# Kernel optimization log

Hardware: AMD Instinct MI355X
Metric: run time of the kernel (lower is better)

Reference implementation:

```python
import jax, jax.numpy as jnp
import numpy as np

N_NODES = 100000
N_EDGES = 1600000
NUM_FEATURES = 64
HIDDEN = 64
NUM_CLASSES = 16


def setup_inputs() -> dict:
    key = jax.random.key(0)
    ks = jax.random.split(key, 8)
    x = jax.random.normal(ks[0], (N_NODES, NUM_FEATURES), dtype=jnp.float32)
    edge_index = jax.random.randint(ks[1], (2, N_EDGES), 0, N_NODES, dtype=jnp.int32)
    # Glorot-ish init for weights, zero bias (matches GCNConv / Linear defaults closely enough)
    s1 = 1.0 / np.sqrt(NUM_FEATURES)
    s2 = 1.0 / np.sqrt(HIDDEN)
    W1 = jax.random.uniform(ks[2], (NUM_FEATURES, HIDDEN), jnp.float32, -s1, s1)
    b1 = jnp.zeros((HIDDEN,), jnp.float32)
    W2 = jax.random.uniform(ks[3], (HIDDEN, HIDDEN), jnp.float32, -s2, s2)
    b2 = jnp.zeros((HIDDEN,), jnp.float32)
    W3 = jax.random.uniform(ks[4], (HIDDEN, NUM_CLASSES), jnp.float32, -s2, s2)
    b3 = jax.random.uniform(ks[5], (NUM_CLASSES,), jnp.float32, -s2, s2)
    return {"x": x, "edge_index": edge_index, "W1": W1, "b1": b1,
            "W2": W2, "b2": b2, "W3": W3, "b3": b3}


def _gcn_layer(x, W, b, src, dst, norm, n_nodes):
    # GCNConv: h = X W; out[i] = sum_{(j->i)} norm_ji * h[j]; out += b
    h = x @ W                                   # [N, H] small dense GEMM
    msg = h[src] * norm[:, None]                # [E+N, H] irregular gather
    out = jax.ops.segment_sum(msg, dst, num_segments=n_nodes)  # scatter-add
    return out + b


def reference(x, edge_index, W1, b1, W2, b2, W3, b3):
    n = x.shape[0]
    loop = jnp.arange(n, dtype=edge_index.dtype)
    # add self-loops (PyG GCNConv default add_self_loops=True)
    src = jnp.concatenate([edge_index[0], loop])
    dst = jnp.concatenate([edge_index[1], loop])
    # symmetric normalization D^{-1/2} A_hat D^{-1/2}
    deg = jax.ops.segment_sum(jnp.ones_like(src, dtype=x.dtype), dst, num_segments=n)
    dis = jax.lax.rsqrt(deg)                    # deg >= 1 due to self-loops
    norm = dis[src] * dis[dst]                  # [E+N]

    h = jax.nn.relu(_gcn_layer(x, W1, b1, src, dst, norm, n))
    # F.dropout(training=False) -> identity (module in eval mode)
    h = jax.nn.relu(_gcn_layer(h, W2, b2, src, dst, norm, n))
    z = h @ W3 + b3
    return jax.nn.log_softmax(z, axis=1), h
```

## Files before the change

kernel.cpp:

```cpp
#include <hip/hip_runtime.h>
#include <hip/hip_bf16.h>

typedef __hip_bfloat16 bf16;
typedef unsigned short ushort;

#define NN 100000
#define NE 1600000
#define NBKT 391
#define BCAP 4608
#define EPB 4096
#define NP1 391
#define NMT 6250

typedef __attribute__((ext_vector_type(8))) short s8v;
typedef __attribute__((ext_vector_type(4))) float f4v;
typedef __attribute__((ext_vector_type(2))) float f2v;

__device__ __forceinline__ float ldf(const void* p, int i, int f32) {
    return f32 ? ((const float*)p)[i] : __bfloat162float(((const bf16*)p)[i]);
}
__device__ __forceinline__ void stf(void* p, int i, int f32, float v) {
    if (f32) ((float*)p)[i] = v;
    else     ((bf16*)p)[i] = __float2bfloat16(v);
}

__device__ __forceinline__ ushort f2b(float f) {
    unsigned u = __builtin_bit_cast(unsigned, f);
    u += 0x7FFF + ((u >> 16) & 1);
    return (ushort)(u >> 16);
}
__device__ __forceinline__ float b2f(ushort h) {
    unsigned u = ((unsigned)h) << 16;
    return __builtin_bit_cast(float, u);
}
__device__ __forceinline__ float blo(unsigned u) {
    return __builtin_bit_cast(float, u << 16);
}
__device__ __forceinline__ float bhi(unsigned u) {
    return __builtin_bit_cast(float, u & 0xffff0000u);
}
__device__ __forceinline__ f2v up2(unsigned u) {
    f2v r; r.x = blo(u); r.y = bhi(u); return r;
}

__global__ void k_sentinel(unsigned* out) {
    if (threadIdx.x == 0 && blockIdx.x == 0) out[0] = 0x461C461Cu;
}

__global__ void k_cnt(const unsigned* __restrict__ x, int* __restrict__ flag,
                      const int* __restrict__ dst, int* __restrict__ cnt) {
    __shared__ int hist[NBKT];
    int b = blockIdx.x, t = threadIdx.x;
    for (int i = t; i < NBKT; i += 256) hist[i] = 0;
    __syncthreads();
    int e0 = b * EPB;
#pragma unroll
    for (int k = 0; k < EPB; k += 256) {
        int e = e0 + k + t;
        if (e < NE) atomicAdd(&hist[dst[e] >> 8], 1);
    }
    __syncthreads();
    for (int i = t; i < NBKT; i += 256) cnt[b * NBKT + i] = hist[i];
    if (b == 0) {
        int c = 0;
        for (int i = t; i < 2048; i += 256) {
            unsigned e7 = (x[i] >> 8) & 0x7F;
            c += (e7 >= 60 && e7 <= 66) ? 1 : 0;
        }
        __syncthreads();
        hist[t] = c;
        __syncthreads();
        for (int s = 128; s > 0; s >>= 1) {
            if (t < s) hist[t] += hist[t + s];
            __syncthreads();
        }
        if (t == 0) *flag = (hist[0] >= 1024) ? 0 : 1;
    }
}

__global__ void k_colscan(const int* __restrict__ cnt, int* __restrict__ prefT,
                          int* __restrict__ btot) {
    __shared__ int s[512];
    int k = blockIdx.x, t = threadIdx.x;
    int v = (t < NP1) ? cnt[t * NBKT + k] : 0;
    s[t] = v;
    __syncthreads();
    for (int d = 1; d < 512; d <<= 1) {
        int add = (t >= d) ? s[t - d] : 0;
        __syncthreads();
        s[t] += add;
        __syncthreads();
    }
    if (t < NP1) prefT[k * NP1 + t] = s[t] - v;
    if (t == 511) btot[k] = s[511];
}

__global__ void __launch_bounds__(512) k_place(
        const int* __restrict__ src, const int* __restrict__ dst,
        const int* __restrict__ prefT, unsigned* __restrict__ bbuf) {
    __shared__ int base[NBKT];
    __shared__ int hist[NBKT];
    __shared__ int lofs[512];
    __shared__ unsigned vals[EPB];
    __shared__ int addr[EPB];
    int b = blockIdx.x, t = threadIdx.x;
    for (int i = t; i < NBKT; i += 512) {
        base[i] = prefT[i * NP1 + b];
        hist[i] = 0;
    }
    __syncthreads();
    int e0 = b * EPB;
    unsigned ev[8];
    int kb[8];
#pragma unroll
    for (int k = 0; k < 8; k++) {
        int e = e0 + k * 512 + t;
        if (e < NE) {
            int d = dst[e];
            ev[k] = ((unsigned)src[e] << 8) | (unsigned)(d & 255);
            kb[k] = d >> 8;
        } else kb[k] = -1;
    }
#pragma unroll
    for (int k = 0; k < 8; k++)
        if (kb[k] >= 0) atomicAdd(&hist[kb[k]], 1);
    __syncthreads();
    int v = (t < NBKT) ? hist[t] : 0;
    lofs[t] = v;
    __syncthreads();
    for (int d = 1; d < 512; d <<= 1) {
        int add = (t >= d) ? lofs[t - d] : 0;
        __syncthreads();
        lofs[t] += add;
        __syncthreads();
    }
    int ex = lofs[t] - v;
    __syncthreads();
    lofs[t] = ex;
    if (t < NBKT) hist[t] = 0;
    __syncthreads();
#pragma unroll
    for (int k = 0; k < 8; k++) {
        if (kb[k] >= 0) {
            int p = atomicAdd(&hist[kb[k]], 1);
            int li = lofs[kb[k]] + p;
            vals[li] = ev[k];
            addr[li] = kb[k] * BCAP + base[kb[k]] + p;
        }
    }
    __syncthreads();
    int tot = min(EPB, NE - e0);
    for (int i = t; i < tot; i += 512) bbuf[addr[i]] = vals[i];
}

__global__ void k_pass2(const unsigned* __restrict__ bbuf, const int* __restrict__ btot,
                        int* __restrict__ rowptr, float* __restrict__ dis,
                        int* __restrict__ csr_off) {
    __shared__ unsigned vals[BCAP];
    __shared__ int lout[BCAP];
    __shared__ int fh[256], fx[256], fc[256];
    int b = blockIdx.x, t = threadIdx.x;
    int part = 0;
    for (int i = t; i < b; i += 256) part += btot[i];
    fh[t] = part;
    __syncthreads();
    for (int s = 128; s > 0; s >>= 1) {
        if (t < s) fh[t] += fh[t + s];
        __syncthreads();
    }
    int g0 = fh[0];
    int cntb = btot[b];
    if (b == 0 && t == 0) rowptr[NN] = NE;
    __syncthreads();
    const unsigned* in = bbuf + b * BCAP;
    fh[t] = 0;
    __syncthreads();
    for (int i = t; i < cntb; i += 256) {
        unsigned v = in[i];
        vals[i] = v;
        atomicAdd(&fh[v & 255], 1);
    }
    __syncthreads();
    fx[t] = fh[t];
    __syncthreads();
    for (int d = 1; d < 256; d <<= 1) {
        int add = (t >= d) ? fx[t - d] : 0;
        __syncthreads();
        fx[t] += add;
        __syncthreads();
    }
    int n = b * 256 + t;
    int ex = fx[t] - fh[t];
    fc[t] = ex;
    if (n < NN) {
        rowptr[n] = g0 + ex;
        dis[n] = rsqrtf(1.0f + (float)fh[t]);
    }
    __syncthreads();
    for (int i = t; i < cntb; i += 256) {
        unsigned v = vals[i];
        int p = atomicAdd(&fc[v & 255], 1);
        lout[p] = (int)((v >> 8) << 7);
    }
    __syncthreads();
    for (int i = t; i < cntb; i += 256) csr_off[g0 + i] = lout[i];
}

__global__ void __launch_bounds__(256) k_gemm_mfma(
        const void* __restrict__ A, int aBase, const void* __restrict__ W,
        bf16* __restrict__ C, const float* __restrict__ dis,
        const int* __restrict__ flag) {
    int f32 = *flag;
    int t = threadIdx.x;
    if (blockIdx.x == 0 && t < 64) ((ushort*)C)[NN * 64 + t] = 0;
    int lane = t & 63;
    int w = t >> 6;
    int m = lane & 15, q = lane >> 4;

    s8v bh[2][4], bl[2][4];
#pragma unroll
    for (int st = 0; st < 2; st++)
#pragma unroll
        for (int nt = 0; nt < 4; nt++)
#pragma unroll
            for (int j = 0; j < 8; j++) {
                int k = st * 32 + q * 8 + j;
                float wv = ldf(W, k * 64 + nt * 16 + m, f32);
                ushort h = f2b(wv);
                bh[st][nt][j] = (short)h;
                bl[st][nt][j] = (short)f2b(wv - b2f(h));
            }

    ushort* Cu = (ushort*)C;
    int gw = blockIdx.x * 4 + w;
    int nw = gridDim.x * 4;
    for (int mt = gw; mt < NMT; mt += nw) {
        int row = mt * 16 + m;
        s8v ah[2], al[2];
        if (f32) {
            const float* ap = (const float*)A + aBase + row * 64 + q * 8;
#pragma unroll
            for (int st = 0; st < 2; st++) {
                f4v va = *(const f4v*)(ap + st * 32);
                f4v vb = *(const f4v*)(ap + st * 32 + 4);
#pragma unroll
                for (int j = 0; j < 8; j++) {
                    float v = (j < 4) ? va[j] : vb[j - 4];
                    ushort h = f2b(v);
                    ah[st][j] = (short)h;
                    al[st][j] = (short)f2b(v - b2f(h));
                }
            }
        } else {
            const short* ap = (const short*)A + aBase + row * 64 + q * 8;
            ah[0] = *(const s8v*)(ap);
            ah[1] = *(const s8v*)(ap + 32);
        }
        float dr[4];
#pragma unroll
        for (int r = 0; r < 4; r++) dr[r] = dis[mt * 16 + q * 4 + r];
#pragma unroll
        for (int nt = 0; nt < 4; nt++) {
            f4v acc = {0.f, 0.f, 0.f, 0.f};
#pragma unroll
            for (int st = 0; st < 2; st++)
                acc = __builtin_amdgcn_mfma_f32_16x16x32_bf16(ah[st], bh[st][nt], acc, 0, 0, 0);
            if (f32) {
#pragma unroll
                for (int st = 0; st < 2; st++) {
                    acc = __builtin_amdgcn_mfma_f32_16x16x32_bf16(ah[st], bl[st][nt], acc, 0, 0, 0);
                    acc = __builtin_amdgcn_mfma_f32_16x16x32_bf16(al[st], bh[st][nt], acc, 0, 0, 0);
                }
            }
            int col = nt * 16 + m;
#pragma unroll
            for (int r = 0; r < 4; r++) {
                int rr = mt * 16 + q * 4 + r;
                Cu[rr * 64 + col] = f2b(dr[r] * acc[r]);
            }
        }
    }
}

__global__ void __launch_bounds__(256, 8) k_aggregate(
        const bf16* __restrict__ hs, void* hout, int hoBase,
        const float* __restrict__ dis,
        const int* __restrict__ rowptr,
        const int* __restrict__ csr_off,
        const void* __restrict__ bias,
        const int* __restrict__ flag) {
    int f32 = *flag;
    int t = threadIdx.x;
    int l = t & 63;
    int q = l >> 4;
    int m = l & 15;
    int fb = m * 8;
    const char* hb = (const char*)hs;
    float b0 = ldf(bias, m * 4 + 0, f32);
    float b1v = ldf(bias, m * 4 + 1, f32);
    float b2v = ldf(bias, m * 4 + 2, f32);
    float b3v = ldf(bias, m * 4 + 3, f32);
    const int Z = NN * 128;
    int wid = blockIdx.x * 4 + (t >> 6);
    int nwav = gridDim.x * 4;
    for (int n = wid; n < NN; n += nwav) {
        int r0 = rowptr[n], r1 = rowptr[n + 1];
        f2v a01 = {0.f, 0.f}, a23 = {0.f, 0.f};
        int j = r0;
        for (; j + 16 <= r1; j += 16) {
            int o0 = csr_off[j + q];
            int o1 = csr_off[j + 4 + q];
            int o2 = csr_off[j + 8 + q];
            int o3 = csr_off[j + 12 + q];
            uint2 v0 = *(const uint2*)(hb + o0 + fb);
            uint2 v1 = *(const uint2*)(hb + o1 + fb);
            uint2 v2 = *(const uint2*)(hb + o2 + fb);
            uint2 v3 = *(const uint2*)(hb + o3 + fb);
            a01 += up2(v0.x); a23 += up2(v0.y);
            a01 += up2(v1.x); a23 += up2(v1.y);
            a01 += up2(v2.x); a23 += up2(v2.y);
            a01 += up2(v3.x); a23 += up2(v3.y);
        }
        if (j < r1) {
            int i0 = j + q, i1 = j + 4 + q, i2 = j + 8 + q, i3 = j + 12 + q;
            int o0 = csr_off[i0]; o0 = (i0 < r1) ? o0 : Z;
            int o1 = csr_off[i1]; o1 = (i1 < r1) ? o1 : Z;
            int o2 = csr_off[i2]; o2 = (i2 < r1) ? o2 : Z;
            int o3 = csr_off[i3]; o3 = (i3 < r1) ? o3 : Z;
            uint2 v0 = *(const uint2*)(hb + o0 + fb);
            uint2 v1 = *(const uint2*)(hb + o1 + fb);
            uint2 v2 = *(const uint2*)(hb + o2 + fb);
            uint2 v3 = *(const uint2*)(hb + o3 + fb);
            a01 += up2(v0.x); a23 += up2(v0.y);
            a01 += up2(v1.x); a23 += up2(v1.y);
            a01 += up2(v2.x); a23 += up2(v2.y);
            a01 += up2(v3.x); a23 += up2(v3.y);
        }
        float a0 = a01.x, a1 = a01.y, a2 = a23.x, a3 = a23.y;
        a0 += __shfl_xor(a0, 32); a1 += __shfl_xor(a1, 32);
        a2 += __shfl_xor(a2, 32); a3 += __shfl_xor(a3, 32);
        a0 += __shfl_xor(a0, 16); a1 += __shfl_xor(a1, 16);
        a2 += __shfl_xor(a2, 16); a3 += __shfl_xor(a3, 16);
        if (q == 0) {
            uint2 sv = *(const uint2*)(hb + n * 128 + fb);
            float dn = dis[n];
            float o0 = fmaxf(dn * (a0 + blo(sv.x)) + b0, 0.f);
            float o1 = fmaxf(dn * (a1 + bhi(sv.x)) + b1v, 0.f);
            float o2 = fmaxf(dn * (a2 + blo(sv.y)) + b2v, 0.f);
            float o3 = fmaxf(dn * (a3 + bhi(sv.y)) + b3v, 0.f);
            if (f32) {
                float4 ov = {o0, o1, o2, o3};
                *(float4*)((float*)hout + hoBase + n * 64 + m * 4) = ov;
            } else {
                unsigned w0 = (unsigned)f2b(o0) | ((unsigned)f2b(o1) << 16);
                unsigned w1 = (unsigned)f2b(o2) | ((unsigned)f2b(o3) << 16);
                uint2 wv; wv.x = w0; wv.y = w1;
                *(uint2*)((ushort*)hout + hoBase + n * 64 + m * 4) = wv;
            }
        }
    }
}

__global__ void k_head(const void* __restrict__ h2, int hBase,
                       const void* __restrict__ W3, const void* __restrict__ b3,
                       void* out, const int* __restrict__ flag) {
    __shared__ float w[64 * 16];
    __shared__ float hrow[64 * 65];
    int f32 = *flag;
    int t = threadIdx.x;
#pragma unroll
    for (int i = 0; i < 4; i++) w[t + i * 256] = ldf(W3, t + i * 256, f32);
    int r0 = blockIdx.x * 64;
#pragma unroll
    for (int i = 0; i < 16; i++) {
        int idx = t + i * 256;
        int row = idx >> 6;
        hrow[row * 65 + (idx & 63)] =
            (r0 + row < NN) ? ldf(h2, hBase + r0 * 64 + idx, f32) : 0.f;
    }
    __syncthreads();
    int lr = t >> 4, c = t & 15;
    float bc = ldf(b3, c, f32);
#pragma unroll
    for (int g = 0; g < 4; g++) {
        int row = lr + g * 16;
        float z = bc;
#pragma unroll
        for (int k = 0; k < 64; k++) z += hrow[row * 65 + k] * w[k * 16 + c];
        float m = z;
#pragma unroll
        for (int off = 8; off >= 1; off >>= 1) m = fmaxf(m, __shfl_xor(m, off, 16));
        float p = __expf(z - m);
        float s = p;
#pragma unroll
        for (int off = 8; off >= 1; off >>= 1) s += __shfl_xor(s, off, 16);
        if (r0 + row < NN)
            stf(out, (r0 + row) * 16 + c, f32, z - m - __logf(s));
    }
}

extern "C" void kernel_launch(void* const* d_in, const int* in_sizes, int n_in,
                              void* d_out, int out_size, void* d_ws, size_t ws_size,
                              hipStream_t stream) {
    const void* x  = d_in[0];
    const int* ei  = (const int*)d_in[1];
    const void* W1 = d_in[2];
    const void* b1 = d_in[3];
    const void* W2 = d_in[4];
    const void* b2 = d_in[5];
    const void* W3 = d_in[6];
    const void* b3 = d_in[7];

    const size_t NEEDED = (size_t)(1807104 + 3203072) * 4;
    if (ws_size < NEEDED) {
        k_sentinel<<<1, 64, 0, stream>>>((unsigned*)d_out);
        return;
    }
    int*      flag    = (int*)d_ws;
    float*    dis     = (float*)d_ws + 256;
    int*      rowptr  = (int*)d_ws + 102656;
    int*      btot    = (int*)d_ws + 205568;
    int*      csr_off = (int*)d_ws + 207104;
    unsigned* bbuf    = (unsigned*)((int*)d_ws + 1807104);
    int*      cnt     = (int*)d_ws + 1807104 + NBKT * BCAP;
    int*      prefT   = cnt + 153088;
    bf16*     bufA    = (bf16*)bbuf;

    const int* srcp = ei;
    const int* dstp = ei + NE;
    const int HB = NN * 16;

    k_cnt<<<NP1, 256, 0, stream>>>((const unsigned*)x, flag, dstp, cnt);
    k_colscan<<<NBKT, 512, 0, stream>>>(cnt, prefT, btot);
    k_place<<<NP1, 512, 0, stream>>>(srcp, dstp, prefT, bbuf);
    k_pass2<<<NBKT, 256, 0, stream>>>(bbuf, btot, rowptr, dis, csr_off);

    k_gemm_mfma<<<1563, 256, 0, stream>>>(x, 0, W1, bufA, dis, flag);
    k_aggregate<<<2048, 256, 0, stream>>>(bufA, d_out, HB, dis, rowptr,
                                          csr_off, b1, flag);

    k_gemm_mfma<<<1563, 256, 0, stream>>>(d_out, HB, W2, bufA, dis, flag);
    k_aggregate<<<2048, 256, 0, stream>>>(bufA, d_out, HB, dis, rowptr,
                                          csr_off, b2, flag);

    k_head<<<1563, 256, 0, stream>>>(d_out, HB, W3, b3, d_out, flag);
}
```

Baseline: 258.0 us.

## Fuse CSR build kernels into one cooperative kernel with grid syncs

Merges the four CSR-construction kernels (count, column scan, place, pass2) into a single cooperative kernel of 391 blocks by 512 threads, using grid.sync() between phases and one shared-memory arena reused across phases. This removes three kernel launches and their inter-kernel gaps. In exchange it adds grid-wide barrier cost, depends on all 391 blocks being co-resident, and runs the count and pass2 phases at 512 threads where they previously used 256.

Result: slower. 406.9 us (+57.7%).

```diff
diff --git a/kernel.cpp b/kernel.cpp
--- a/kernel.cpp
+++ b/kernel.cpp
@@ -1,5 +1,8 @@
 #include <hip/hip_runtime.h>
 #include <hip/hip_bf16.h>
+#include <hip/hip_cooperative_groups.h>
+
+namespace cg = cooperative_groups;
 
 typedef __hip_bfloat16 bf16;
 typedef unsigned short ushort;
@@ -47,163 +50,169 @@
     if (threadIdx.x == 0 && blockIdx.x == 0) out[0] = 0x461C461Cu;
 }
 
-__global__ void k_cnt(const unsigned* __restrict__ x, int* __restrict__ flag,
-                      const int* __restrict__ dst, int* __restrict__ cnt) {
-    __shared__ int hist[NBKT];
+__global__ void __launch_bounds__(512) k_csr(
+        const unsigned* __restrict__ x, int* __restrict__ flag,
+        const int* __restrict__ src, const int* __restrict__ dst,
+        int* __restrict__ cnt, int* __restrict__ prefT, int* __restrict__ btot,
+        unsigned* __restrict__ bbuf, int* __restrict__ rowptr,
+        float* __restrict__ dis, int* __restrict__ csr_off) {
+    __shared__ int smem[10240];
+    cg::grid_group grid = cg::this_grid();
     int b = blockIdx.x, t = threadIdx.x;
-    for (int i = t; i < NBKT; i += 256) hist[i] = 0;
-    __syncthreads();
     int e0 = b * EPB;
-#pragma unroll
-    for (int k = 0; k < EPB; k += 256) {
-        int e = e0 + k + t;
-        if (e < NE) atomicAdd(&hist[dst[e] >> 8], 1);
-    }
-    __syncthreads();
-    for (int i = t; i < NBKT; i += 256) cnt[b * NBKT + i] = hist[i];
-    if (b == 0) {
-        int c = 0;
-        for (int i = t; i < 2048; i += 256) {
-            unsigned e7 = (x[i] >> 8) & 0x7F;
-            c += (e7 >= 60 && e7 <= 66) ? 1 : 0;
-        }
-        __syncthreads();
-        hist[t] = c;
-        __syncthreads();
-        for (int s = 128; s > 0; s >>= 1) {
-            if (t < s) hist[t] += hist[t + s];
-            __syncthreads();
-        }
-        if (t == 0) *flag = (hist[0] >= 1024) ? 0 : 1;
-    }
-}
-
-__global__ void k_colscan(const int* __restrict__ cnt, int* __restrict__ prefT,
-                          int* __restrict__ btot) {
-    __shared__ int s[512];
-    int k = blockIdx.x, t = threadIdx.x;
-    int v = (t < NP1) ? cnt[t * NBKT + k] : 0;
-    s[t] = v;
-    __syncthreads();
-    for (int d = 1; d < 512; d <<= 1) {
-        int add = (t >= d) ? s[t - d] : 0;
-        __syncthreads();
-        s[t] += add;
-        __syncthreads();
-    }
-    if (t < NP1) prefT[k * NP1 + t] = s[t] - v;
-    if (t == 511) btot[k] = s[511];
-}
-
-__global__ void __launch_bounds__(512) k_place(
-        const int* __restrict__ src, const int* __restrict__ dst,
-        const int* __restrict__ prefT, unsigned* __restrict__ bbuf) {
-    __shared__ int base[NBKT];
-    __shared__ int hist[NBKT];
-    __shared__ int lofs[512];
-    __shared__ unsigned vals[EPB];
-    __shared__ int addr[EPB];
-    int b = blockIdx.x, t = threadIdx.x;
-    for (int i = t; i < NBKT; i += 512) {
-        base[i] = prefT[i * NP1 + b];
-        hist[i] = 0;
-    }
-    __syncthreads();
-    int e0 = b * EPB;
-    unsigned ev[8];
-    int kb[8];
-#pragma unroll
-    for (int k = 0; k < 8; k++) {
-        int e = e0 + k * 512 + t;
-        if (e < NE) {
-            int d = dst[e];
-            ev[k] = ((unsigned)src[e] << 8) | (unsigned)(d & 255);
-            kb[k] = d >> 8;
-        } else kb[k] = -1;
-    }
-#pragma unroll
-    for (int k = 0; k < 8; k++)
-        if (kb[k] >= 0) atomicAdd(&hist[kb[k]], 1);
-    __syncthreads();
-    int v = (t < NBKT) ? hist[t] : 0;
-    lofs[t] = v;
-    __syncthreads();
-    for (int d = 1; d < 512; d <<= 1) {
-        int add = (t >= d) ? lofs[t - d] : 0;
-        __syncthreads();
-        lofs[t] += add;
-        __syncthreads();
-    }
-    int ex = lofs[t] - v;
-    __syncthreads();
-    lofs[t] = ex;
-    if (t < NBKT) hist[t] = 0;
-    __syncthreads();
-#pragma unroll
-    for (int k = 0; k < 8; k++) {
-        if (kb[k] >= 0) {
-            int p = atomicAdd(&hist[kb[k]], 1);
-            int li = lofs[kb[k]] + p;
-            vals[li] = ev[k];
-            addr[li] = kb[k] * BCAP + base[kb[k]] + p;
-        }
-    }
-    __syncthreads();
-    int tot = min(EPB, NE - e0);
-    for (int i = t; i < tot; i += 512) bbuf[addr[i]] = vals[i];
-}
-
-__global__ void k_pass2(const unsigned* __restrict__ bbuf, const int* __restrict__ btot,
-                        int* __restrict__ rowptr, float* __restrict__ dis,
-                        int* __restrict__ csr_off) {
-    __shared__ unsigned vals[BCAP];
-    __shared__ int lout[BCAP];
-    __shared__ int fh[256], fx[256], fc[256];
-    int b = blockIdx.x, t = threadIdx.x;
-    int part = 0;
-    for (int i = t; i < b; i += 256) part += btot[i];
-    fh[t] = part;
-    __syncthreads();
-    for (int s = 128; s > 0; s >>= 1) {
-        if (t < s) fh[t] += fh[t + s];
-        __syncthreads();
-    }
-    int g0 = fh[0];
-    int cntb = btot[b];
-    if (b == 0 && t == 0) rowptr[NN] = NE;
-    __syncthreads();
-    const unsigned* in = bbuf + b * BCAP;
-    fh[t] = 0;
-    __syncthreads();
-    for (int i = t; i < cntb; i += 256) {
-        unsigned v = in[i];
-        vals[i] = v;
-        atomicAdd(&fh[v & 255], 1);
-    }
-    __syncthreads();
-    fx[t] = fh[t];
-    __syncthreads();
-    for (int d = 1; d < 256; d <<= 1) {
-        int add = (t >= d) ? fx[t - d] : 0;
-        __syncthreads();
-        fx[t] += add;
-        __syncthreads();
-    }
-    int n = b * 256 + t;
-    int ex = fx[t] - fh[t];
-    fc[t] = ex;
-    if (n < NN) {
-        rowptr[n] = g0 + ex;
-        dis[n] = rsqrtf(1.0f + (float)fh[t]);
-    }
-    __syncthreads();
-    for (int i = t; i < cntb; i += 256) {
-        unsigned v = vals[i];
-        int p = atomicAdd(&fc[v & 255], 1);
-        lout[p] = (int)((v >> 8) << 7);
-    }
-    __syncthreads();
-    for (int i = t; i < cntb; i += 256) csr_off[g0 + i] = lout[i];
+
+    {
+        int* hist = smem;
+        for (int i = t; i < NBKT; i += 512) hist[i] = 0;
+        __syncthreads();
+        for (int k = 0; k < EPB; k += 512) {
+            int e = e0 + k + t;
+            if (e < NE) atomicAdd(&hist[dst[e] >> 8], 1);
+        }
+        __syncthreads();
+        for (int i = t; i < NBKT; i += 512) cnt[b * NBKT + i] = hist[i];
+        if (b == 0) {
+            int* dc = smem + 512;
+            int c = 0;
+            for (int i = t; i < 2048; i += 512) {
+                unsigned e7 = (x[i] >> 8) & 0x7F;
+                c += (e7 >= 60 && e7 <= 66) ? 1 : 0;
+            }
+            dc[t] = c;
+            __syncthreads();
+            for (int s = 256; s > 0; s >>= 1) {
+                if (t < s) dc[t] += dc[t + s];
+                __syncthreads();
+            }
+            if (t == 0) *flag = (dc[0] >= 1024) ? 0 : 1;
+        }
+    }
+    grid.sync();
+
+    {
+        int* s = smem;
+        int v = (t < NP1) ? cnt[t * NBKT + b] : 0;
+        s[t] = v;
+        __syncthreads();
+        for (int d = 1; d < 512; d <<= 1) {
+            int add = (t >= d) ? s[t - d] : 0;
+            __syncthreads();
+            s[t] += add;
+            __syncthreads();
+        }
+        if (t < NP1) prefT[b * NP1 + t] = s[t] - v;
+        if (t == 511) btot[b] = s[511];
+    }
+    grid.sync();
+
+    {
+        int* base = smem;
+        int* hcur = smem + 400;
+        int* lofs = smem + 800;
+        unsigned* vals = (unsigned*)(smem + 1312);
+        int* addr = smem + 5408;
+        for (int i = t; i < NBKT; i += 512) {
+            base[i] = prefT[i * NP1 + b];
+            hcur[i] = 0;
+        }
+        __syncthreads();
+        unsigned ev[8];
+        int kb[8];
+#pragma unroll
+        for (int k = 0; k < 8; k++) {
+            int e = e0 + k * 512 + t;
+            if (e < NE) {
+                int d = dst[e];
+                ev[k] = ((unsigned)src[e] << 8) | (unsigned)(d & 255);
+                kb[k] = d >> 8;
+            } else kb[k] = -1;
+        }
+#pragma unroll
+        for (int k = 0; k < 8; k++)
+            if (kb[k] >= 0) atomicAdd(&hcur[kb[k]], 1);
+        __syncthreads();
+        int v = (t < NBKT) ? hcur[t] : 0;
+        lofs[t] = v;
+        __syncthreads();
+        for (int d = 1; d < 512; d <<= 1) {
+            int add = (t >= d) ? lofs[t - d] : 0;
+            __syncthreads();
+            lofs[t] += add;
+            __syncthreads();
+        }
+        int ex = lofs[t] - v;
+        __syncthreads();
+        lofs[t] = ex;
+        if (t < NBKT) hcur[t] = 0;
+        __syncthreads();
+#pragma unroll
+        for (int k = 0; k < 8; k++) {
+            if (kb[k] >= 0) {
+                int p = atomicAdd(&hcur[kb[k]], 1);
+                int li = lofs[kb[k]] + p;
+                vals[li] = ev[k];
+                addr[li] = kb[k] * BCAP + base[kb[k]] + p;
+            }
+        }
+        __syncthreads();
+        int tot = min(EPB, NE - e0);
+        for (int i = t; i < tot; i += 512) bbuf[addr[i]] = vals[i];
+    }
+    grid.sync();
+
+    {
+        unsigned* vals = (unsigned*)smem;
+        int* lout = smem + 4608;
+        int* fh = smem + 9216;
+        int* fx = smem + 9472;
+        int* fc = smem + 9728;
+        int part = 0;
+        for (int i = t; i < b; i += 512) part += btot[i];
+        lout[t] = part;
+        __syncthreads();
+        for (int s = 256; s > 0; s >>= 1) {
+            if (t < s) lout[t] += lout[t + s];
+            __syncthreads();
+        }
+        int g0 = lout[0];
+        int cntb = btot[b];
+        if (b == 0 && t == 0) rowptr[NN] = NE;
+        __syncthreads();
+        const unsigned* in = bbuf + b * BCAP;
+        if (t < 256) fh[t] = 0;
+        __syncthreads();
+        for (int i = t; i < cntb; i += 512) {
+            unsigned v = in[i];
+            vals[i] = v;
+            atomicAdd(&fh[v & 255], 1);
+        }
+        __syncthreads();
+        if (t < 256) fx[t] = fh[t];
+        __syncthreads();
+        for (int d = 1; d < 256; d <<= 1) {
+            int add = (t < 256 && t >= d) ? fx[t - d] : 0;
+            __syncthreads();
+            if (t < 256) fx[t] += add;
+            __syncthreads();
+        }
+        if (t < 256) {
+            int n = b * 256 + t;
+            int ex = fx[t] - fh[t];
+            fc[t] = ex;
+            if (n < NN) {
+                rowptr[n] = g0 + ex;
+                dis[n] = rsqrtf(1.0f + (float)fh[t]);
+            }
+        }
+        __syncthreads();
+        for (int i = t; i < cntb; i += 512) {
+            unsigned v = vals[i];
+            int p = atomicAdd(&fc[v & 255], 1);
+            lout[p] = (int)((v >> 8) << 7);
+        }
+        __syncthreads();
+        for (int i = t; i < cntb; i += 512) csr_off[g0 + i] = lout[i];
+    }
 }
 
 __global__ void __launch_bounds__(256) k_gemm_mfma(
@@ -430,10 +439,12 @@
     const int* dstp = ei + NE;
     const int HB = NN * 16;
 
-    k_cnt<<<NP1, 256, 0, stream>>>((const unsigned*)x, flag, dstp, cnt);
-    k_colscan<<<NBKT, 512, 0, stream>>>(cnt, prefT, btot);
-    k_place<<<NP1, 512, 0, stream>>>(srcp, dstp, prefT, bbuf);
-    k_pass2<<<NBKT, 256, 0, stream>>>(bbuf, btot, rowptr, dis, csr_off);
+    const unsigned* xu = (const unsigned*)x;
+    void* csr_args[] = { (void*)&xu, (void*)&flag, (void*)&srcp, (void*)&dstp,
+                         (void*)&cnt, (void*)&prefT, (void*)&btot, (void*)&bbuf,
+                         (void*)&rowptr, (void*)&dis, (void*)&csr_off };
+    hipLaunchCooperativeKernel((const void*)k_csr, dim3(NP1), dim3(512),
+                               csr_args, 0, stream);
 
     k_gemm_mfma<<<1563, 256, 0, stream>>>(x, 0, W1, bufA, dis, flag);
     k_aggregate<<<2048, 256, 0, stream>>>(bufA, d_out, HB, dis, rowptr,
```
